# Optimization experiments

Measured on AMD Instinct MI355X. Metric: run time of the kernel, lower is better.

Reference implementation:

```python
import jax, jax.numpy as jnp
import numpy as np

NG = 6      # K*2 graphs
N = 6000    # nodes per graph
E = 96000   # edges per graph
F_IN = 128  # input node feature dim
C = 128     # ggnn_args['out_channels']
BINS = 21


def setup_inputs() -> dict:
    key = jax.random.key(0)
    ks = jax.random.split(key, 5)
    x = jax.random.normal(ks[0], (NG, N, F_IN), jnp.float32)
    edge_index = jax.random.randint(ks[1], (NG, 2, E), 0, N, dtype=jnp.int64)
    edge_attr = jax.random.uniform(ks[2], (NG, E, 6), dtype=jnp.float32)
    # 4 GCNConv layers: Linear (no bias inside lin) + separate bias param
    gcn_W = jax.random.normal(ks[3], (4, F_IN, C), jnp.float32) / np.sqrt(F_IN)
    gcn_b = jnp.zeros((4, C), jnp.float32)
    # 4 xavier-init Ws matrices
    Ws = jax.random.normal(ks[4], (4, C, C), jnp.float32) / np.sqrt(C)
    return {"x": x, "edge_index": edge_index, "edge_attr": edge_attr,
            "gcn_W": gcn_W, "gcn_b": gcn_b, "Ws": Ws}


def _gcn(x, row, col, w, W, b):
    """PyG GCNConv with edge weights: add self-loops (weight 1), symmetric norm."""
    n = x.shape[0]
    loop = jnp.arange(n)
    r = jnp.concatenate([row, loop])
    c = jnp.concatenate([col, loop])
    ww = jnp.concatenate([w, jnp.ones((n,), w.dtype)])
    deg = jax.ops.segment_sum(ww, c, num_segments=n)
    dis = jnp.where(deg > 0, jax.lax.rsqrt(jnp.maximum(deg, 1e-30)), 0.0)
    norm = dis[r] * ww * dis[c]
    h = x @ W  # [n, C]
    out = jax.ops.segment_sum(norm[:, None] * h[r], c, num_segments=n)
    return out + b


def _gnn_layer(x, ei, ea, gcn_W, gcn_b, Ws):
    row, col = ei[0], ei[1]
    acc = jnp.zeros((x.shape[0], C), x.dtype)
    for i in range(4):  # fixed small structural loop
        h = jax.nn.relu(_gcn(x, row, col, ea[:, i + 2], gcn_W[i], gcn_b[i]))
        acc = acc + h @ Ws[i]
    return acc


def reference(x, edge_index, edge_attr, gcn_W, gcn_b, Ws):
    # per-graph GNN features [NG, N, C]
    feats = jax.vmap(lambda xi, ei, ea: _gnn_layer(xi, ei, ea, gcn_W, gcn_b, Ws))(
        x, edge_index, edge_attr)
    # g_matrix: concat of per-graph mean embeddings -> [1, NG*C]
    g_matrix = feats.mean(axis=1).reshape(1, NG * C)
    # L2-normalize rows (F.normalize, eps=1e-12)
    nrm = jnp.linalg.norm(feats, axis=-1, keepdims=True)
    xn = feats / jnp.maximum(nrm, 1e-12)
    centers = jnp.linspace(-1.0, 1.0, BINS, dtype=jnp.float32)  # -1.0 .. 1.0 step 0.1
    width = 2.0 / BINS  # histc bin width over [-1, 1]
    rows = []
    for i1 in range(NG):
        vals = []
        for i2 in range(NG):
            t = jnp.tanh(xn[i1] @ xn[i2].T)  # [N, N]
            idx = jnp.clip(jnp.floor((t + 1.0) / width), 0, BINS - 1).astype(jnp.int32)
            hist = jnp.bincount(idx.ravel(), length=BINS).astype(jnp.float32)
            hist = hist / (N * N)
            vals.append(jnp.dot(hist, centers))
        rows.append(jnp.stack(vals))
    sim_matrix = jnp.stack(rows)[None]  # [1, NG, NG]
    return g_matrix, sim_matrix
```

## Files before the change

kernel.cpp:

```cpp
#include <hip/hip_runtime.h>

#define NG 6
#define NN 6000
#define NE 96000
#define NP2 6144

typedef unsigned int uint;
typedef unsigned short ushort;
typedef unsigned char uchar;
typedef __attribute__((ext_vector_type(8))) short short8;
typedef __attribute__((ext_vector_type(8))) int int8v;
typedef __attribute__((ext_vector_type(4))) float f32x4;
typedef __attribute__((ext_vector_type(2))) float f32x2;

__device__ __forceinline__ ushort f2bf(float f){
  uint u = __float_as_uint(f);
  u = (u + 0x7fffu + ((u >> 16) & 1u)) >> 16;
  return (ushort)u;
}
__device__ __forceinline__ float bf2f(uint u){ return __uint_as_float(u << 16); }

__device__ __forceinline__ void async16(const void* g, void* l){
  __builtin_amdgcn_global_load_lds(
      (const __attribute__((address_space(1))) unsigned int*)g,
      (__attribute__((address_space(3))) unsigned int*)l, 16, 0, 0);
}

__device__ __constant__ int c_i1[21] = {0,0,0,0,0,0,1,1,1,1,1,2,2,2,2,3,3,3,4,4,5};
__device__ __constant__ int c_i2[21] = {0,1,2,3,4,5,1,2,3,4,5,2,3,4,5,3,4,5,4,5,5};
__device__ __constant__ int c_nd[15] = {1,2,3,4,5,7,8,9,10,12,13,14,16,17,19};
__device__ __constant__ int c_dg[6]  = {0,6,11,15,18,20};
__device__ __constant__ int c_dcum[25] = {0,6,12,18,24,29,34,39,44,48,52,56,60,
                                          63,66,69,72,74,76,78,80,81,82,83,84};

__device__ __forceinline__ void stage128s(const ushort* __restrict__ gsrc, int stride,
                                          ushort* lds, int w, int lane){
  #pragma unroll
  for (int i = 0; i < 8; i++){
    int off = (w*8 + i) * 512;
    int rowi = (w*8 + i)*4 + (lane >> 4);
    int chunk = (lane & 15) ^ (rowi & 15);
    async16(gsrc + (size_t)rowi*stride + chunk*8, (void*)&lds[off]);
  }
}

__device__ __forceinline__ void stage8(const uchar* __restrict__ gsrc,
                                       uchar* lds, int w, int lane){
  #pragma unroll
  for (int j = 0; j < 2; j++){
    int cj = w*2 + j;
    int d = cj*64 + lane;
    int row = d >> 3, slot = d & 7;
    async16(gsrc + (size_t)row*128 + ((slot ^ (row & 7)) << 4),
            (void*)(lds + cj*1024));
  }
}

__device__ __forceinline__ void mfma128(const ushort* As, const ushort* Bs,
                                        int w, int lane, f32x4 acc[4][4]){
  int q = lane >> 4, cl = lane & 15;
  int wm = w >> 1, wn = w & 1;
  #pragma unroll
  for (int ks = 0; ks < 4; ks++){
    short8 af[4], bfr[4];
    int ch = ((ks*4 + q) ^ cl) * 8;
    #pragma unroll
    for (int m = 0; m < 4; m++) af[m]  = *(const short8*)&As[(wm*64 + m*16 + cl)*128 + ch];
    #pragma unroll
    for (int n = 0; n < 4; n++) bfr[n] = *(const short8*)&Bs[(wn*64 + n*16 + cl)*128 + ch];
    #pragma unroll
    for (int m = 0; m < 4; m++)
      #pragma unroll
      for (int n = 0; n < 4; n++)
        acc[m][n] = __builtin_amdgcn_mfma_f32_16x16x32_bf16(af[m], bfr[n], acc[m][n], 0, 0, 0);
  }
}
__device__ __forceinline__ void zacc(f32x4 acc[4][4]){
  #pragma unroll
  for (int m = 0; m < 4; m++)
    #pragma unroll
    for (int n = 0; n < 4; n++) acc[m][n] = (f32x4){0.f,0.f,0.f,0.f};
}

#define TC1 10.499108f
#define TC3 (-3.4888668f)
#define TC5 1.3464888f
#define TC7 (-0.4433517f)
#define TC9 0.0833385f
__device__ __forceinline__ f32x2 psumT(const f32x4 acc[4][4]){
  f32x2 t2 = {0.f, 0.f};
  #pragma unroll
  for (int m = 0; m < 4; m++)
    #pragma unroll
    for (int n = 0; n < 4; n++)
      #pragma unroll
      for (int rp = 0; rp < 2; rp++){
        f32x2 d = { acc[m][n][rp*2], acc[m][n][rp*2+1] };
        f32x2 t = d*d;
        f32x2 qq = t*TC9 + TC7;
        qq = qq*t + TC5;
        qq = qq*t + TC3;
        qq = qq*t + TC1;
        t2 = d*qq + t2;
      }
  return t2;
}

__global__ void k_zero4(float4* p, int n16){
  int i = blockIdx.x*256 + threadIdx.x;
  if (i < n16) p[i] = make_float4(0.f,0.f,0.f,0.f);
}
__global__ void k_zero1(float* p, int n){
  int i = blockIdx.x*256 + threadIdx.x;
  if (i < n) p[i] = 0.f;
}
__global__ void k_cvtx(const float4* x, uint2* xbf, int n4){
  int i = blockIdx.x*256 + threadIdx.x;
  if (i >= n4) return;
  float4 v = x[i];
  xbf[i] = make_uint2((uint)f2bf(v.x) | ((uint)f2bf(v.y) << 16),
                      (uint)f2bf(v.z) | ((uint)f2bf(v.w) << 16));
}
__global__ void k_cvt_w(const float* W, const float* Wsm, ushort* Wtc, ushort* Wstc){
  int i = blockIdx.x*256 + threadIdx.x;
  int l = i >> 14, rem = i & 16383;
  int a = rem >> 7, b = rem & 127;
  Wtc[(l << 14) + b*128 + a] = f2bf(W[i]);
  Wstc[b*512 + l*128 + a]    = f2bf(Wsm[i]);
}
__global__ void k_count(const int* ei, int* counts){
  int i = blockIdx.x*256 + threadIdx.x;
  if (i >= NG*NE) return;
  int g = i / NE, e = i - g*NE;
  atomicAdd(&counts[g*NN + ei[g*2*NE + NE + e]], 1);
}
__global__ void k_scan(const int* counts, int* offs, int* cursor){
  __shared__ int sm[256];
  int g = blockIdx.x, t = threadIdx.x;
  const int* c = counts + g*NN;
  int i0 = t*24, i1 = i0 + 24; if (i1 > NN) i1 = NN; if (i0 > NN) i0 = NN;
  int s = 0;
  for (int i = i0; i < i1; i++) s += c[i];
  sm[t] = s;
  __syncthreads();
  for (int off = 1; off < 256; off <<= 1){
    int v = (t >= off) ? sm[t - off] : 0;
    __syncthreads();
    sm[t] += v;
    __syncthreads();
  }
  int run = sm[t] - s;
  for (int i = i0; i < i1; i++){
    offs[g*NN + i] = run; cursor[g*NN + i] = run; run += c[i];
  }
}
__global__ void k_place(const int* ei, int* cursor, int2* elist2){
  int i = blockIdx.x*256 + threadIdx.x;
  if (i >= NG*NE) return;
  int g = i / NE, e = i - g*NE;
  int col = ei[g*2*NE + NE + e];
  int row = ei[g*2*NE + e];
  int pos = atomicAdd(&cursor[g*NN + col], 1);
  elist2[g*NE + pos] = make_int2(e, row);
}
__global__ void k_deg(const float* __restrict__ ea, const int* __restrict__ offs,
                      const int* __restrict__ counts, const int2* __restrict__ elist2,
                      float4* __restrict__ dis4){
  int i = blockIdx.x*256 + threadIdx.x;
  if (i >= NG*NN) return;
  int g = i / NN;
  int beg = offs[i], cnt = counts[i];
  const int2* el = elist2 + (size_t)g*NE;
  const float* eag = ea + (size_t)g*NE*6;
  float4 s = make_float4(1.f,1.f,1.f,1.f);
  for (int j = 0; j < cnt; j++){
    int e = el[beg + j].x;
    float2 wa = *(const float2*)(eag + (size_t)e*6 + 2);
    float2 wb = *(const float2*)(eag + (size_t)e*6 + 4);
    s.x += wa.x; s.y += wa.y; s.z += wb.x; s.w += wb.y;
  }
  dis4[i] = make_float4(rsqrtf(fmaxf(s.x,1e-30f)), rsqrtf(fmaxf(s.y,1e-30f)),
                        rsqrtf(fmaxf(s.z,1e-30f)), rsqrtf(fmaxf(s.w,1e-30f)));
}

__global__ __launch_bounds__(256) void k_gather1(const float* __restrict__ ea,
    const float4* __restrict__ dis4, const int* __restrict__ offs,
    const int* __restrict__ counts, const int2* __restrict__ elist2,
    const ushort* __restrict__ xbf, ushort* __restrict__ agg, int c){
  __shared__ int    sr[4][64];
  __shared__ float4 sc[4][64];
  int lane = threadIdx.x, wy = threadIdx.y;
  int nidx = blockIdx.x*4 + wy;
  int lg = nidx / NN, n = nidx - lg*NN;
  int g = c*2 + lg;
  float4 dn4 = dis4[g*NN + n];
  const uint* xrow = (const uint*)xbf + (size_t)lg*NN*64;
  uint xv = xrow[(size_t)n*64 + lane];
  f32x2 xs = {bf2f(xv & 0xffffu), bf2f(xv >> 16)};
  f32x2 a0 = xs*dn4.x, a1 = xs*dn4.y, a2 = xs*dn4.z, a3 = xs*dn4.w;
  int beg = offs[g*NN + n], cnt = counts[g*NN + n];
  const int2*  el  = elist2 + (size_t)g*NE;
  const float* eag = ea + (size_t)g*NE*6;
  for (int j0 = 0; j0 < cnt; j0 += 64){
    int take = cnt - j0; if (take > 64) take = 64;
    if (lane < take){
      int2 er = el[beg + j0 + lane];
      float2 wa = *(const float2*)(eag + (size_t)er.x*6 + 2);
      float2 wb = *(const float2*)(eag + (size_t)er.x*6 + 4);
      float4 dr = dis4[g*NN + er.y];
      sr[wy][lane] = er.y;
      sc[wy][lane] = make_float4(wa.x*dr.x, wa.y*dr.y, wb.x*dr.z, wb.y*dr.w);
    }
    int j = 0;
    for (; j + 4 <= take; j += 4){
      int r0 = sr[wy][j], r1 = sr[wy][j+1], r2 = sr[wy][j+2], r3 = sr[wy][j+3];
      float4 c0 = sc[wy][j], c1 = sc[wy][j+1], c2 = sc[wy][j+2], c3 = sc[wy][j+3];
      uint x0 = xrow[(size_t)r0*64 + lane];
      uint x1 = xrow[(size_t)r1*64 + lane];
      uint x2 = xrow[(size_t)r2*64 + lane];
      uint x3 = xrow[(size_t)r3*64 + lane];
      f32x2 v;
      v = (f32x2){bf2f(x0 & 0xffffu), bf2f(x0 >> 16)};
      a0 = v*c0.x + a0; a1 = v*c0.y + a1; a2 = v*c0.z + a2; a3 = v*c0.w + a3;
      v = (f32x2){bf2f(x1 & 0xffffu), bf2f(x1 >> 16)};
      a0 = v*c1.x + a0; a1 = v*c1.y + a1; a2 = v*c1.z + a2; a3 = v*c1.w + a3;
      v = (f32x2){bf2f(x2 & 0xffffu), bf2f(x2 >> 16)};
      a0 = v*c2.x + a0; a1 = v*c2.y + a1; a2 = v*c2.z + a2; a3 = v*c2.w + a3;
      v = (f32x2){bf2f(x3 & 0xffffu), bf2f(x3 >> 16)};
      a0 = v*c3.x + a0; a1 = v*c3.y + a1; a2 = v*c3.z + a2; a3 = v*c3.w + a3;
    }
    for (; j < take; j++){
      int r0 = sr[wy][j];
      float4 c0 = sc[wy][j];
      uint x0 = xrow[(size_t)r0*64 + lane];
      f32x2 v = (f32x2){bf2f(x0 & 0xffffu), bf2f(x0 >> 16)};
      a0 = v*c0.x + a0; a1 = v*c0.y + a1; a2 = v*c0.z + a2; a3 = v*c0.w + a3;
    }
  }
  a0 = a0*dn4.x; a1 = a1*dn4.y; a2 = a2*dn4.z; a3 = a3*dn4.w;
  uint* ag = (uint*)agg;
  ag[((size_t)((lg*4+0)*NN + n))*64 + lane] = (uint)f2bf(a0.x) | ((uint)f2bf(a0.y) << 16);
  ag[((size_t)((lg*4+1)*NN + n))*64 + lane] = (uint)f2bf(a1.x) | ((uint)f2bf(a1.y) << 16);
  ag[((size_t)((lg*4+2)*NN + n))*64 + lane] = (uint)f2bf(a2.x) | ((uint)f2bf(a2.y) << 16);
  ag[((size_t)((lg*4+3)*NN + n))*64 + lane] = (uint)f2bf(a3.x) | ((uint)f2bf(a3.y) << 16);
}

__global__ __launch_bounds__(256) void k_gemm1b(const ushort* __restrict__ agg,
    const ushort* __restrict__ Wtc, const float* __restrict__ gb,
    ushort* __restrict__ H){
  __shared__ ushort As[16384];
  __shared__ ushort Bsh[16384];
  int by = blockIdx.y;
  int lg = by >> 2, l = by & 3;
  int tid = threadIdx.x, w = tid >> 6, lane = tid & 63;
  stage128s(agg + (size_t)by*NN*128 + (size_t)blockIdx.x*16384, 128, As, w, lane);
  stage128s(Wtc + (l << 14), 128, Bsh, w, lane);
  __syncthreads();
  f32x4 acc[4][4];
  zacc(acc);
  mfma128(As, Bsh, w, lane, acc);
  int q = lane >> 4, cl = lane & 15, wm = w >> 1, wn = w & 1;
  int rowb = blockIdx.x*128 + wm*64 + q*4;
  int colb = wn*64 + cl;
  #pragma unroll
  for (int m = 0; m < 4; m++)
    #pragma unroll
    for (int n = 0; n < 4; n++)
      #pragma unroll
      for (int r = 0; r < 4; r++){
        int row = rowb + m*16 + r, col = colb + n*16;
        if (row < NN){
          float v = fmaxf(acc[m][n][r] + gb[l*128 + col], 0.f);
          H[((size_t)(lg*NN + row))*512 + l*128 + col] = f2bf(v);
        }
      }
}

__global__ __launch_bounds__(256) void k_gemm2(const ushort* __restrict__ A,
    const ushort* __restrict__ B, float* __restrict__ feats, int coff){
  __shared__ ushort As[16384];
  __shared__ ushort Bsh[16384];
  int tid = threadIdx.x, w = tid >> 6, lane = tid & 63;
  f32x4 acc[4][4];
  zacc(acc);
  #pragma unroll
  for (int kc = 0; kc < 4; kc++){
    if (kc) __syncthreads();
    stage128s(A + (size_t)blockIdx.x*128*512 + kc*128, 512, As, w, lane);
    stage128s(B + kc*128, 512, Bsh, w, lane);
    __syncthreads();
    mfma128(As, Bsh, w, lane, acc);
  }
  int q = lane >> 4, cl = lane & 15, wm = w >> 1, wn = w & 1;
  int rowb = blockIdx.x*128 + wm*64 + q*4;
  int colb = wn*64 + cl;
  #pragma unroll
  for (int m = 0; m < 4; m++)
    #pragma unroll
    for (int n = 0; n < 4; n++)
      #pragma unroll
      for (int r = 0; r < 4; r++){
        int row = rowb + m*16 + r;
        if (row < 2*NN)
          feats[(size_t)(coff + row)*128 + colb + n*16] = acc[m][n][r];
      }
}

__global__ void k_mean(const float* feats, float* out){
  int g = blockIdx.x / 48, ch = blockIdx.x - g*48;
  int c = threadIdx.x;
  float s = 0.f;
  int n0 = ch*125;
  for (int n = n0; n < n0 + 125; n++) s += feats[((size_t)(g*NN + n))*128 + c];
  atomicAdd(&out[g*128 + c], s * (1.0f/6000.0f));
}

__global__ void k_xn(const float* feats, uchar* xn8){
  int lane = threadIdx.x;
  int rall = blockIdx.x*4 + threadIdx.y;
  int g = rall / NP2, rl = rall - g*NP2;
  ushort* dst = (ushort*)(xn8 + ((size_t)(g*NP2 + rl))*128);
  if (rl < NN){
    const float2* src = (const float2*)&feats[((size_t)(g*NN + rl))*128];
    float2 v = src[lane];
    float ss = v.x*v.x + v.y*v.y;
    #pragma unroll
    for (int s = 32; s > 0; s >>= 1) ss += __shfl_xor(ss, s);
    float inv = 1.0f / fmaxf(sqrtf(ss), 1e-12f);
    int pk = __builtin_amdgcn_cvt_pk_fp8_f32(v.x*inv, v.y*inv, 0, false);
    dst[lane] = (ushort)(pk & 0xffff);
  } else {
    dst[lane] = 0;
  }
}

__global__ __launch_bounds__(256, 3) void k_pair(const uchar* __restrict__ xn8,
                                                 float* Spart){
  __shared__ uchar Bs[2][8192];
  int bx = blockIdx.x;
  int p, rt, c0, niter; bool diag;
  if (bx < 2160){
    int pp = bx / 144, rem = bx - pp*144;
    rt = rem / 6; int ch = rem - rt*6;
    p = c_nd[pp]; diag = false; c0 = ch*16; niter = 16;
  } else {
    int idd = bx - 2160;
    int pd = idd / 84, rem = idd - pd*84;
    int r_ = 0;
    while (c_dcum[r_ + 1] <= rem) r_++;
    rt = r_;
    int ch = rem - c_dcum[rt];
    p = c_dg[pd]; diag = true;
    c0 = 4*rt + ch*16;
    int left = 96 - c0;
    niter = left < 16 ? left : 16;
  }
  int i1 = c_i1[p], i2 = c_i2[p];
  int tid = threadIdx.x, w = tid >> 6, lane = tid & 63;
  int q = lane >> 4, cl = lane & 15;
  const uchar* Arow = xn8 + ((size_t)i1*NP2 + rt*256 + w*64 + cl)*128 + q*32;
  int8v afr[4];
  #pragma unroll
  for (int m = 0; m < 4; m++){
    uint4 lo = *(const uint4*)(Arow + m*2048);
    uint4 hi = *(const uint4*)(Arow + m*2048 + 16);
    afr[m] = (int8v){(int)lo.x,(int)lo.y,(int)lo.z,(int)lo.w,
                     (int)hi.x,(int)hi.y,(int)hi.z,(int)hi.w};
  }
  int b0 = cl*128 + (((q*2  ) ^ (cl & 7)) << 4);
  int b1 = cl*128 + (((q*2+1) ^ (cl & 7)) << 4);
  const uchar* Bbase = xn8 + (size_t)i2*NP2*128;
  stage8(Bbase + (size_t)c0*8192, Bs[0], w, lane);
  f32x2 totw = {0.f, 0.f};
  const f32x4 z4 = {0.f,0.f,0.f,0.f};
  for (int it = 0; it < niter; it++){
    int cur = it & 1;
    __syncthreads();
    if (it + 1 < niter)
      stage8(Bbase + (size_t)(c0+it+1)*8192, Bs[1-cur], w, lane);
    __builtin_amdgcn_s_setprio(1);
    int8v bfr[4];
    #pragma unroll
    for (int n = 0; n < 4; n++){
      uint4 lo = *(const uint4*)&Bs[cur][b0 + n*2048];
      uint4 hi = *(const uint4*)&Bs[cur][b1 + n*2048];
      bfr[n] = (int8v){(int)lo.x,(int)lo.y,(int)lo.z,(int)lo.w,
                       (int)hi.x,(int)hi.y,(int)hi.z,(int)hi.w};
    }
    f32x4 acc[4][4];
    #pragma unroll
    for (int m = 0; m < 4; m++)
      #pragma unroll
      for (int n = 0; n < 4; n++)
        acc[m][n] = __builtin_amdgcn_mfma_scale_f32_16x16x128_f8f6f4(
            afr[m], bfr[n], z4, 0, 0, 0, 0x7F, 0, 0x7F);
    __builtin_amdgcn_s_setprio(0);
    f32x2 t2 = psumT(acc);
    float wgt = (diag && (c0 + it) >= 4*rt + 4) ? 2.f : 1.f;
    totw = t2*wgt + totw;
  }
  float tot = totw.x + totw.y;
  #pragma unroll
  for (int s = 32; s > 0; s >>= 1) tot += __shfl_xor(tot, s);
  if (lane == 0) atomicAdd(&Spart[p*64 + (bx & 63)], tot);
}

__global__ void k_final(const float* Spart, float* out){
  int t = threadIdx.x;
  if (t < 21){
    float s = 0.f;
    for (int j = 0; j < 64; j++) s += Spart[t*64 + j];
    float v = s * (1.0f/360000000.0f);
    int i1 = c_i1[t], i2 = c_i2[t];
    out[768 + i1*6 + i2] = v;
    out[768 + i2*6 + i1] = v;
  }
}

extern "C" void kernel_launch(void* const* d_in, const int* in_sizes, int n_in,
                              void* d_out, int out_size, void* d_ws, size_t ws_size,
                              hipStream_t stream){
  (void)in_sizes; (void)n_in; (void)out_size; (void)ws_size;
  const float* x   = (const float*)d_in[0];
  const int*   ei  = (const int*)d_in[1];
  const float* ea  = (const float*)d_in[2];
  const float* gW  = (const float*)d_in[3];
  const float* gb  = (const float*)d_in[4];
  const float* Wsm = (const float*)d_in[5];
  float* out = (float*)d_out;
  char* ws = (char*)d_ws;
  float*  feats  = (float*) (ws + 0);
  int*    counts = (int*)   (ws + 18432000);
  int*    offs   = (int*)   (ws + 18576000);
  int*    cursor = (int*)   (ws + 18720000);
  float*  Spart  = (float*) (ws + 18864000);
  float4* dis4   = (float4*)(ws + 18872192);
  int2*   elist2 = (int2*)  (ws + 19448192);
  ushort* Wtc    = (ushort*)(ws + 24056192);
  ushort* Wstc   = (ushort*)(ws + 24187264);
  ushort* xbf    = (ushort*)(ws + 24318336);
  ushort* agg    = (ushort*)(ws + 27394560);
  ushort* H      = (ushort*)(ws + 39690752);
  uchar*  xn8    = (uchar*) (ws + 24318336);

  k_zero4<<<dim3(108), dim3(256), 0, stream>>>((float4*)(ws + 18432000), 27512);
  k_zero1<<<dim3(4),   dim3(256), 0, stream>>>(out, 804);
  k_cvt_w<<<dim3(256), dim3(256), 0, stream>>>(gW, Wsm, Wtc, Wstc);
  k_count<<<dim3(2250), dim3(256), 0, stream>>>(ei, counts);
  k_scan <<<dim3(6),    dim3(256), 0, stream>>>(counts, offs, cursor);
  k_place<<<dim3(2250), dim3(256), 0, stream>>>(ei, cursor, elist2);
  k_deg  <<<dim3(141),  dim3(256), 0, stream>>>(ea, offs, counts, elist2, dis4);
  for (int c = 0; c < 3; c++){
    k_cvtx   <<<dim3(1500), dim3(256), 0, stream>>>(
        (const float4*)(x + (size_t)c*2*NN*128), (uint2*)xbf, 384000);
    k_gather1<<<dim3(3000), dim3(64,4), 0, stream>>>(ea, dis4, offs, counts, elist2,
                                                     xbf, agg, c);
    k_gemm1b <<<dim3(47,8), dim3(256), 0, stream>>>(agg, Wtc, gb, H);
    k_gemm2  <<<dim3(94),   dim3(256), 0, stream>>>(H, Wstc, feats, c*2*NN);
  }
  k_mean <<<dim3(288),  dim3(128),  0, stream>>>(feats, out);
  k_xn   <<<dim3(9216), dim3(64,4), 0, stream>>>(feats, xn8);
  k_pair <<<dim3(2664), dim3(256),  0, stream>>>(xn8, Spart);
  k_final<<<dim3(1),    dim3(64),   0, stream>>>(Spart, out);
}
```

Measured before the change: 470.3 us.

## Fuse GCN linear and Ws projection GEMMs, keeping hidden tile in LDS

```diff
diff --git a/kernel.cpp b/kernel.cpp
--- a/kernel.cpp
+++ b/kernel.cpp
@@ -245,64 +245,53 @@
   ag[((size_t)((lg*4+3)*NN + n))*64 + lane] = (uint)f2bf(a3.x) | ((uint)f2bf(a3.y) << 16);
 }
 
-__global__ __launch_bounds__(256) void k_gemm1b(const ushort* __restrict__ agg,
+__global__ __launch_bounds__(256, 2) void k_gemmf(const ushort* __restrict__ agg,
     const ushort* __restrict__ Wtc, const float* __restrict__ gb,
-    ushort* __restrict__ H){
+    const ushort* __restrict__ Wstc, float* __restrict__ feats, int coff){
   __shared__ ushort As[16384];
   __shared__ ushort Bsh[16384];
-  int by = blockIdx.y;
-  int lg = by >> 2, l = by & 3;
+  int bx = blockIdx.x;
+  int lg = blockIdx.y;
   int tid = threadIdx.x, w = tid >> 6, lane = tid & 63;
-  stage128s(agg + (size_t)by*NN*128 + (size_t)blockIdx.x*16384, 128, As, w, lane);
-  stage128s(Wtc + (l << 14), 128, Bsh, w, lane);
-  __syncthreads();
-  f32x4 acc[4][4];
-  zacc(acc);
-  mfma128(As, Bsh, w, lane, acc);
   int q = lane >> 4, cl = lane & 15, wm = w >> 1, wn = w & 1;
-  int rowb = blockIdx.x*128 + wm*64 + q*4;
+  int rowb_l = wm*64 + q*4;
   int colb = wn*64 + cl;
+  f32x4 accf[4][4];
+  zacc(accf);
+  #pragma unroll 1
+  for (int l = 0; l < 4; l++){
+    if (l) __syncthreads();
+    stage128s(agg + (size_t)(lg*4+l)*NN*128 + (size_t)bx*16384, 128, As, w, lane);
+    stage128s(Wtc + (l << 14), 128, Bsh, w, lane);
+    __syncthreads();
+    f32x4 acc[4][4];
+    zacc(acc);
+    mfma128(As, Bsh, w, lane, acc);
+    __syncthreads();
+    #pragma unroll
+    for (int m = 0; m < 4; m++)
+      #pragma unroll
+      for (int n = 0; n < 4; n++)
+        #pragma unroll
+        for (int r = 0; r < 4; r++){
+          int row = rowb_l + m*16 + r;
+          int col = colb + n*16;
+          float v = fmaxf(acc[m][n][r] + gb[l*128 + col], 0.f);
+          As[row*128 + (((col >> 3) ^ (row & 15)) << 3) + (col & 7)] = f2bf(v);
+        }
+    stage128s(Wstc + l*128, 512, Bsh, w, lane);
+    __syncthreads();
+    mfma128(As, Bsh, w, lane, accf);
+  }
   #pragma unroll
   for (int m = 0; m < 4; m++)
     #pragma unroll
     for (int n = 0; n < 4; n++)
       #pragma unroll
       for (int r = 0; r < 4; r++){
-        int row = rowb + m*16 + r, col = colb + n*16;
-        if (row < NN){
-          float v = fmaxf(acc[m][n][r] + gb[l*128 + col], 0.f);
-          H[((size_t)(lg*NN + row))*512 + l*128 + col] = f2bf(v);
-        }
-      }
-}
-
-__global__ __launch_bounds__(256) void k_gemm2(const ushort* __restrict__ A,
-    const ushort* __restrict__ B, float* __restrict__ feats, int coff){
-  __shared__ ushort As[16384];
-  __shared__ ushort Bsh[16384];
-  int tid = threadIdx.x, w = tid >> 6, lane = tid & 63;
-  f32x4 acc[4][4];
-  zacc(acc);
-  #pragma unroll
-  for (int kc = 0; kc < 4; kc++){
-    if (kc) __syncthreads();
-    stage128s(A + (size_t)blockIdx.x*128*512 + kc*128, 512, As, w, lane);
-    stage128s(B + kc*128, 512, Bsh, w, lane);
-    __syncthreads();
-    mfma128(As, Bsh, w, lane, acc);
-  }
-  int q = lane >> 4, cl = lane & 15, wm = w >> 1, wn = w & 1;
-  int rowb = blockIdx.x*128 + wm*64 + q*4;
-  int colb = wn*64 + cl;
-  #pragma unroll
-  for (int m = 0; m < 4; m++)
-    #pragma unroll
-    for (int n = 0; n < 4; n++)
-      #pragma unroll
-      for (int r = 0; r < 4; r++){
-        int row = rowb + m*16 + r;
-        if (row < 2*NN)
-          feats[(size_t)(coff + row)*128 + colb + n*16] = acc[m][n][r];
+        int grow = bx*128 + rowb_l + m*16 + r;
+        if (grow < NN)
+          feats[(size_t)(coff + lg*NN + grow)*128 + colb + n*16] = accf[m][n][r];
       }
 }
 
@@ -440,7 +429,6 @@
   ushort* Wstc   = (ushort*)(ws + 24187264);
   ushort* xbf    = (ushort*)(ws + 24318336);
   ushort* agg    = (ushort*)(ws + 27394560);
-  ushort* H      = (ushort*)(ws + 39690752);
   uchar*  xn8    = (uchar*) (ws + 24318336);
 
   k_zero4<<<dim3(108), dim3(256), 0, stream>>>((float4*)(ws + 18432000), 27512);
@@ -455,8 +443,7 @@
         (const float4*)(x + (size_t)c*2*NN*128), (uint2*)xbf, 384000);
     k_gather1<<<dim3(3000), dim3(64,4), 0, stream>>>(ea, dis4, offs, counts, elist2,
                                                      xbf, agg, c);
-    k_gemm1b <<<dim3(47,8), dim3(256), 0, stream>>>(agg, Wtc, gb, H);
-    k_gemm2  <<<dim3(94),   dim3(256), 0, stream>>>(H, Wstc, feats, c*2*NN);
+    k_gemmf  <<<dim3(47,2), dim3(256), 0, stream>>>(agg, Wtc, gb, Wstc, feats, c*2*NN);
   }
   k_mean <<<dim3(288),  dim3(128),  0, stream>>>(feats, out);
   k_xn   <<<dim3(9216), dim3(64,4), 0, stream>>>(feats, xn8);
```

Result: slower. 540.5 us (+14.9%).
